# Kernel optimization log

Hardware: AMD Instinct MI355X
Metric: run time of the kernel (lower is better)

Reference implementation:

```python
import jax, jax.numpy as jnp
import numpy as np

N, F = 4096, 256  # nodes, in_features == hidden_features == out_features; num_heads = 1
LN_EPS = 1e-5
L1_EPS = 1e-12


def setup_inputs() -> dict:
    key = jax.random.key(0)
    k0, k1, k2, k3, k4 = jax.random.split(key, 5)
    h = jax.random.normal(k0, (N, F), jnp.float32)
    x = jax.random.normal(k1, (N, F), jnp.float32)
    s = 1.0 / np.sqrt(F)
    s_v = 1.0 / np.sqrt(F + 3)
    # torch Linear weight layout: [out_features, in_features]
    w_k = jax.random.uniform(k2, (F, F), jnp.float32, -s, s)
    w_q = jax.random.uniform(k3, (F, F), jnp.float32, -s, s)
    w_v = jax.random.uniform(k4, (F, F + 3), jnp.float32, -s_v, s_v)
    # mixing init: ones * semantic_weight(-1.0), row 0 zeroed
    mixing = jnp.full((2, 2), -1.0, jnp.float32).at[0].set(0.0)
    ln_gamma = jnp.ones((F,), jnp.float32)
    ln_beta = jnp.zeros((F,), jnp.float32)
    return {"h": h, "x": x, "w_k": w_k, "w_q": w_q, "w_v": w_v,
            "mixing": mixing, "ln_gamma": ln_gamma, "ln_beta": ln_beta}


def reference(h, x, w_k, w_q, w_v, mixing, ln_gamma, ln_beta):
    h0, x0 = h, x
    # LayerNorm (biased variance, eps=1e-5)
    mu = h.mean(-1, keepdims=True)
    var = ((h - mu) ** 2).mean(-1, keepdims=True)
    hn = (h - mu) * jax.lax.rsqrt(var + LN_EPS) * ln_gamma + ln_beta
    # F.normalize(x, p=1): divide by max(L1 norm, eps)
    xn = x / jnp.maximum(jnp.abs(x).sum(-1, keepdims=True), L1_EPS)
    # projections (single head: [N, F])
    k = hn @ w_k.T
    q = hn @ w_q.T
    # feature-attention: softmax over last dim of k q^T / sqrt(F)
    a_h = jax.nn.softmax((k @ q.T) * (F ** -0.5), axis=-1)          # [N, N]
    # x-affinity
    a_x = xn @ xn.T                                                  # [N, N]
    # stats of a_x rows: diag, sum, std (unbiased, ddof=1)
    i = jnp.stack([jnp.diagonal(a_x), a_x.sum(-1), a_x.std(-1, ddof=1)], axis=-1)  # [N, 3]
    # learned 2x2 mixing, softmax over dim 0 (columns)
    m = jax.nn.softmax(mixing, axis=0)
    a_x2 = a_x * m[0, 0] + a_h * m[1, 0]
    a_h2 = a_x * m[0, 1] + a_h * m[1, 1]
    # torch a_h.transpose(-1, 0) swaps the row axis with the head axis,
    # transposing the NxN matrix (head dim = 1): h <- a_h2^T @ hn
    h_agg = a_h2.T @ hn                                              # [N, F]
    x_out = a_x2 @ xn                                                # [N, F]
    h_out = jax.nn.elu(jnp.concatenate([h_agg, i], axis=-1) @ w_v.T)
    return (h_out + h0, x_out + x0)
```

## Files before the change

kernel.cpp:

```cpp
#include <hip/hip_runtime.h>
#include <cstdint>
#include <cstddef>

#define NB 4096
#define FD 256

typedef __attribute__((ext_vector_type(4))) float f32x4;
typedef __attribute__((ext_vector_type(8))) short bf16x8;

__device__ __forceinline__ ushort f2bf(float f) {
  union { float f; uint32_t u; } v; v.f = f;
  uint32_t r = v.u + 0x7fffu + ((v.u >> 16) & 1u);
  return (ushort)(r >> 16);
}
__device__ __forceinline__ float bf2f(ushort b) {
  union { uint32_t u; float f; } v; v.u = ((uint32_t)b) << 16;
  return v.f;
}

__device__ __forceinline__ void gld16(const void* g, void* l) {
  __builtin_amdgcn_global_load_lds(
      (const __attribute__((address_space(1))) char*)g,
      (__attribute__((address_space(3))) char*)l, 16, 0, 0);
}

__device__ __forceinline__ float wave_reduce_sum(float v) {
#pragma unroll
  for (int off = 32; off >= 1; off >>= 1) v += __shfl_xor(v, off);
  return v;
}
__device__ __forceinline__ float wave_reduce_max(float v) {
#pragma unroll
  for (int off = 32; off >= 1; off >>= 1) v = fmaxf(v, __shfl_xor(v, off));
  return v;
}

__global__ __launch_bounds__(256) void rownorm_kernel(
    const float* __restrict__ h, const float* __restrict__ x,
    const float* __restrict__ gamma, const float* __restrict__ beta,
    ushort* __restrict__ hnb, ushort* __restrict__ xnb, float* __restrict__ diag) {
  __shared__ float rA[4], rB[4], rC[4], rD[4];
  const int r = blockIdx.x, t = threadIdx.x, wid = t >> 6, lane = t & 63;
  const size_t base = (size_t)r * FD + t;
  const float hv = h[base], xv = x[base];
  float s1 = wave_reduce_sum(hv);
  float s2 = wave_reduce_sum(hv * hv);
  float a1 = wave_reduce_sum(fabsf(xv));
  float q1 = wave_reduce_sum(xv * xv);
  if (lane == 0) { rA[wid] = s1; rB[wid] = s2; rC[wid] = a1; rD[wid] = q1; }
  __syncthreads();
  const float S1 = rA[0] + rA[1] + rA[2] + rA[3];
  const float S2 = rB[0] + rB[1] + rB[2] + rB[3];
  const float L1 = rC[0] + rC[1] + rC[2] + rC[3];
  const float Q1 = rD[0] + rD[1] + rD[2] + rD[3];
  const float mu = S1 * (1.0f / FD);
  const float var = S2 * (1.0f / FD) - mu * mu;
  const float rstd = rsqrtf(var + 1e-5f);
  const float d = fmaxf(L1, 1e-12f), dinv = 1.0f / d;
  hnb[base] = f2bf((hv - mu) * rstd * gamma[t] + beta[t]);
  xnb[base] = f2bf(xv * dinv);
  if (t == 0) diag[r] = Q1 * dinv * dinv;
}

__global__ __launch_bounds__(256) void wcast_kernel(
    const float* __restrict__ w_k, const float* __restrict__ w_q,
    const float* __restrict__ w_v,
    ushort* __restrict__ wkqb, ushort* __restrict__ wvAb,
    float* __restrict__ wvbT3) {
  const int r = blockIdx.x, t = threadIdx.x;
  wkqb[r * 256 + t] = f2bf(w_k[r * 256 + t]);
  wkqb[(256 + r) * 256 + t] = f2bf(w_q[r * 256 + t]);
  wvAb[r * 256 + t] = f2bf(w_v[(size_t)r * 259 + t]);
  if (t < 3) wvbT3[t * 256 + r] = w_v[(size_t)r * 259 + 256 + t];
}

__global__ __launch_bounds__(256) void transpose2_kernel(
    const ushort* __restrict__ inA, ushort* __restrict__ outA,
    const ushort* __restrict__ inB, ushort* __restrict__ outB, int R, int C) {
  __shared__ ushort tile[64][65];
  const ushort* in = blockIdx.z ? inB : inA;
  ushort* out = blockIdx.z ? outB : outA;
  const int bc = blockIdx.x * 64, br = blockIdx.y * 64;
  const int t = threadIdx.x;
#pragma unroll
  for (int i = 0; i < 16; ++i) {
    const int idx = t + 256 * i;
    const int rr = idx >> 6, cc = idx & 63;
    tile[rr][cc] = in[(size_t)(br + rr) * C + bc + cc];
  }
  __syncthreads();
#pragma unroll
  for (int i = 0; i < 16; ++i) {
    const int idx = t + 256 * i;
    const int rr = idx >> 6, cc = idx & 63;
    out[(size_t)(bc + rr) * R + br + cc] = tile[cc][rr];
  }
}

__global__ __launch_bounds__(256) void transpose_kernel(
    const ushort* __restrict__ in, ushort* __restrict__ out, int R, int C) {
  __shared__ ushort tile[64][65];
  const int bc = blockIdx.x * 64, br = blockIdx.y * 64;
  const int t = threadIdx.x;
#pragma unroll
  for (int i = 0; i < 16; ++i) {
    const int idx = t + 256 * i;
    const int rr = idx >> 6, cc = idx & 63;
    tile[rr][cc] = in[(size_t)(br + rr) * C + bc + cc];
  }
  __syncthreads();
#pragma unroll
  for (int i = 0; i < 16; ++i) {
    const int idx = t + 256 * i;
    const int rr = idx >> 6, cc = idx & 63;
    out[(size_t)(bc + rr) * R + br + cc] = tile[cc][rr];
  }
}

__global__ __launch_bounds__(256) void colsum_kernel(
    const ushort* __restrict__ xnT, float* __restrict__ s) {
  __shared__ float red[4];
  const int f = blockIdx.x, t = threadIdx.x, wid = t >> 6, lane = t & 63;
  float a = 0.f;
#pragma unroll
  for (int i = 0; i < 16; ++i) a += bf2f(xnT[(size_t)f * NB + t + 256 * i]);
  a = wave_reduce_sum(a);
  if (lane == 0) red[wid] = a;
  __syncthreads();
  if (t == 0) s[f] = red[0] + red[1] + red[2] + red[3];
}

__global__ __launch_bounds__(256) void reduce16g_kernel(
    const float* __restrict__ in, ushort* __restrict__ t23B,
    ushort* __restrict__ M2T) {
  const int idx = blockIdx.x * 256 + threadIdx.x;
  const int i = idx >> 9, j = idx & 511;
  float a = 0.f;
#pragma unroll
  for (int z = 0; z < 16; ++z) a += in[(size_t)z * (256 * 512) + idx];
  if (j < 256) t23B[i * 256 + j] = f2bf(a);
  else M2T[i * 256 + (j - 256)] = f2bf(a);
}

__global__ __launch_bounds__(256) void softmax_kernel(
    const ushort* __restrict__ S, ushort* __restrict__ P) {
  __shared__ float red[4];
  const int r = blockIdx.x, t = threadIdx.x, wid = t >> 6, lane = t & 63;
  const uint4* Sr = (const uint4*)(S + (size_t)r * NB);
  float v[16];
  float lmax = -1e30f;
#pragma unroll
  for (int i = 0; i < 2; ++i) {
    const uint4 c = Sr[t + 256 * i];
    const uint32_t w4[4] = {c.x, c.y, c.z, c.w};
#pragma unroll
    for (int j = 0; j < 4; ++j) {
      v[i * 8 + j * 2]     = bf2f((ushort)(w4[j] & 0xffffu));
      v[i * 8 + j * 2 + 1] = bf2f((ushort)(w4[j] >> 16));
    }
  }
#pragma unroll
  for (int u = 0; u < 16; ++u) lmax = fmaxf(lmax, v[u]);
  lmax = wave_reduce_max(lmax);
  if (lane == 0) red[wid] = lmax;
  __syncthreads();
  const float gmax = fmaxf(fmaxf(red[0], red[1]), fmaxf(red[2], red[3]));
  __syncthreads();
  float lsum = 0.f;
#pragma unroll
  for (int u = 0; u < 16; ++u) { v[u] = __expf(v[u] - gmax); lsum += v[u]; }
  lsum = wave_reduce_sum(lsum);
  if (lane == 0) red[wid] = lsum;
  __syncthreads();
  const float pinv = 1.f / (red[0] + red[1] + red[2] + red[3]);
  uint4* Pr = (uint4*)(P + (size_t)r * NB);
#pragma unroll
  for (int i = 0; i < 2; ++i) {
    uint4 o;
    o.x = (uint32_t)f2bf(v[i*8+0] * pinv) | ((uint32_t)f2bf(v[i*8+1] * pinv) << 16);
    o.y = (uint32_t)f2bf(v[i*8+2] * pinv) | ((uint32_t)f2bf(v[i*8+3] * pinv) << 16);
    o.z = (uint32_t)f2bf(v[i*8+4] * pinv) | ((uint32_t)f2bf(v[i*8+5] * pinv) << 16);
    o.w = (uint32_t)f2bf(v[i*8+6] * pinv) | ((uint32_t)f2bf(v[i*8+7] * pinv) << 16);
    Pr[t + 256 * i] = o;
  }
}

__global__ __launch_bounds__(256) void megacombine_kernel(
    const ushort* __restrict__ px, const ushort* __restrict__ ph,
    const float* __restrict__ t23, const ushort* __restrict__ xnb,
    const float* __restrict__ sv, const float* __restrict__ diag,
    const float* __restrict__ x, const float* __restrict__ h,
    const float* __restrict__ wvbT3, const float* __restrict__ mix,
    float* __restrict__ out_x, float* __restrict__ out_h) {
  __shared__ float rA[4], rB[4];
  const size_t NF = (size_t)NB * FD;
  const int i = blockIdx.x, f = threadIdx.x, wid = f >> 6, lane = f & 63;
  const float e0x = __expf(mix[0]), e1x = __expf(mix[2]);
  const float mAx = e0x / (e0x + e1x), mBx = e1x / (e0x + e1x);
  const float e0h = __expf(mix[1]), e1h = __expf(mix[3]);
  const float mAh = e0h / (e0h + e1h), mBh = e1h / (e0h + e1h);

  const size_t rowoff = (size_t)i * FD + f;
  float ax = 0.f, ah = 0.f;
#pragma unroll
  for (int z = 0; z < 8; ++z) {
    ax += bf2f(px[(size_t)z * NF + rowoff]);
    ah += bf2f(ph[(size_t)z * NF + rowoff]);
  }
  const float t2v = t23[(size_t)i * 512 + f];
  const float t3v = t23[(size_t)i * 512 + 256 + f];
  const float xv = bf2f(xnb[rowoff]);

  float rs = wave_reduce_sum(xv * sv[f]);
  float rq = wave_reduce_sum(xv * t2v);
  if (lane == 0) { rA[wid] = rs; rB[wid] = rq; }
  __syncthreads();
  rs = rA[0] + rA[1] + rA[2] + rA[3];
  rq = rB[0] + rB[1] + rB[2] + rB[3];
  const float mean = rs * (1.0f / NB);
  const float var = (rq - (float)NB * mean * mean) * (1.0f / (NB - 1));
  const float sd = sqrtf(fmaxf(var, 0.f));
  const float dg = diag[i];
  const float statsterm = dg * wvbT3[f] + rs * wvbT3[256 + f] + sd * wvbT3[512 + f];

  out_x[rowoff] = mBx * ax + mAx * t2v + x[rowoff];
  const float pre = mBh * ah + mAh * t3v + statsterm;
  out_h[rowoff] = ((pre > 0.f) ? pre : expm1f(pre)) + h[rowoff];
}

template <int BM, int BN, int EPI>
__global__ __launch_bounds__(256) void gemm_nt(
    const ushort* __restrict__ A, int lda,
    const ushort* __restrict__ B, int ldb,
    void* __restrict__ Cp, int ldc, int K, float alpha,
    size_t pstride) {
  constexpr int WAVES_N = (BM <= 32) ? 4 : 2;
  constexpr int WAVES_M = 4 / WAVES_N;
  constexpr int WM = BM / WAVES_M, WN = BN / WAVES_N;
  constexpr int MR = WM / 16, NR = WN / 16;
  __shared__ __align__(16) ushort At[2][BM][32];
  __shared__ __align__(16) ushort Bt[2][BN][32];
  const int tid = threadIdx.x;
  const int wave = tid >> 6, lane = tid & 63;
  const int wr = wave / WAVES_N, wc = wave % WAVES_N;

  const int gx = gridDim.x, gy = gridDim.y;
  const int nwg = gx * gy * gridDim.z;
  int flat = blockIdx.x + gx * (blockIdx.y + gy * blockIdx.z);
  if ((nwg & 7) == 0) flat = (flat & 7) * (nwg >> 3) + (flat >> 3);
  const int bx = flat % gx, by = (flat / gx) % gy, bz = flat / (gx * gy);

  const int bi = by * BM, bj = bx * BN;
  const int fr = lane & 15, fq = lane >> 4;
  const int sub = lane >> 2, q = lane & 3;

  f32x4 acc[MR][NR];
#pragma unroll
  for (int m = 0; m < MR; ++m)
#pragma unroll
    for (int n = 0; n < NR; ++n) acc[m][n] = (f32x4){0.f, 0.f, 0.f, 0.f};

  const int kbase = (EPI >= 5) ? bz * K : 0;
  const int kend = kbase + K;

  auto stage = [&](int bufi, int k0) {
    for (int c = wave; c < BM / 16; c += 4) {
      const int row = c * 16 + sub;
      const int qs = q ^ (row & 3);
      gld16(A + (size_t)(bi + row) * lda + k0 + qs * 8, &At[bufi][c * 16][0]);
    }
    for (int c = wave; c < BN / 16; c += 4) {
      const int row = c * 16 + sub;
      const int qs = q ^ (row & 3);
      gld16(B + (size_t)(bj + row) * ldb + k0 + qs * 8, &Bt[bufi][c * 16][0]);
    }
  };

  stage(0, kbase);
  __syncthreads();

  int cur = 0;
  for (int k0 = kbase; k0 < kend; k0 += 32) {
    if (k0 + 32 < kend) stage(cur ^ 1, k0 + 32);
    bf16x8 a[MR], b[NR];
#pragma unroll
    for (int m = 0; m < MR; ++m) {
      const int row = wr * WM + m * 16 + fr;
      a[m] = *(const bf16x8*)((const char*)&At[cur][row][0] + ((fq ^ (row & 3)) * 16));
    }
#pragma unroll
    for (int n = 0; n < NR; ++n) {
      const int row = wc * WN + n * 16 + fr;
      b[n] = *(const bf16x8*)((const char*)&Bt[cur][row][0] + ((fq ^ (row & 3)) * 16));
    }
#pragma unroll
    for (int m = 0; m < MR; ++m)
#pragma unroll
      for (int n = 0; n < NR; ++n)
        acc[m][n] = __builtin_amdgcn_mfma_f32_16x16x32_bf16(a[m], b[n], acc[m][n], 0, 0, 0);
    __syncthreads();
    cur ^= 1;
  }

#pragma unroll
  for (int m = 0; m < MR; ++m)
#pragma unroll
    for (int n = 0; n < NR; ++n)
#pragma unroll
      for (int r = 0; r < 4; ++r) {
        const int row = bi + wr * WM + m * 16 + fq * 4 + r;
        const int col = bj + wc * WN + n * 16 + fr;
        const size_t ci = (size_t)row * ldc + col;
        const float v = acc[m][n][r];
        if (EPI == 0) ((float*)Cp)[ci] = v * alpha;
        else if (EPI == 1) ((ushort*)Cp)[ci] = f2bf(v * alpha);
        else if (EPI == 5) ((float*)Cp)[(size_t)bz * pstride + ci] = v;
        else if (EPI == 6) ((ushort*)Cp)[(size_t)bz * pstride + ci] = f2bf(v);
      }
}

extern "C" void kernel_launch(void* const* d_in, const int* in_sizes, int n_in,
                              void* d_out, int out_size, void* d_ws, size_t ws_size,
                              hipStream_t stream) {
  const float* h      = (const float*)d_in[0];
  const float* x      = (const float*)d_in[1];
  const float* w_k    = (const float*)d_in[2];
  const float* w_q    = (const float*)d_in[3];
  const float* w_v    = (const float*)d_in[4];
  const float* mixing = (const float*)d_in[5];
  const float* gamma  = (const float*)d_in[6];
  const float* beta   = (const float*)d_in[7];

  float* out_h = (float*)d_out;
  float* out_x = out_h + (size_t)NB * FD;

  char* w = (char*)d_ws;
  ushort* S     = (ushort*)(w + 0);
  ushort* P     = (ushort*)(w + 33554432);
  ushort* PT    = (ushort*)(w + 67108864);
  ushort* hnb   = (ushort*)(w + 100663296);
  ushort* xnb   = (ushort*)(w + 102760448);
  ushort* xnbT  = (ushort*)(w + 104857600);
  ushort* hnbT  = (ushort*)(w + 106954752);
  ushort* kq    = (ushort*)(w + 109051904);
  ushort* hvT   = (ushort*)(w + 113246208);
  float*  t23   = (float*)(w + 115343360);
  ushort* t23B  = (ushort*)(w + 123731968);
  ushort* M2T   = (ushort*)(w + 123994112);
  ushort* wkqb  = (ushort*)(w + 124125184);
  ushort* wvAb  = (ushort*)(w + 124387328);
  float*  wvbT3 = (float*)(w + 124518400);
  float*  diag  = (float*)(w + 124521472);
  float*  sv    = (float*)(w + 124537856);
  float*  Gramp = (float*)(w + 67108864);
  ushort* px    = (ushort*)(w + 0);
  ushort* ph    = (ushort*)(w + 16777216);

  rownorm_kernel<<<NB, 256, 0, stream>>>(h, x, gamma, beta, hnb, xnb, diag);
  wcast_kernel<<<FD, 256, 0, stream>>>(w_k, w_q, w_v, wkqb, wvAb, wvbT3);
  transpose2_kernel<<<dim3(FD / 64, NB / 64, 2), 256, 0, stream>>>(
      xnb, xnbT, hnb, hnbT, NB, FD);
  colsum_kernel<<<FD, 256, 0, stream>>>(xnbT, sv);

  gemm_nt<64, 64, 1><<<dim3(512 / 64, NB / 64), 256, 0, stream>>>(
      hnb, FD, wkqb, FD, kq, 512, FD, 1.f, 0);

  gemm_nt<64, 64, 5><<<dim3(512 / 64, 256 / 64, 16), 256, 0, stream>>>(
      xnbT, NB, xnbT, NB, Gramp, 512, NB / 16, 1.f, (size_t)256 * 512);
  reduce16g_kernel<<<256 * 512 / 256, 256, 0, stream>>>(Gramp, t23B, M2T);

  gemm_nt<64, 64, 1><<<dim3(4, 4), 256, 0, stream>>>(
      wvAb, FD, M2T, FD, t23B + 256 * 256, FD, FD, 1.f, 0);

  gemm_nt<64, 64, 1><<<dim3(NB / 64, FD / 64), 256, 0, stream>>>(
      wvAb, FD, hnb, FD, hvT, NB, FD, 1.f, 0);

  gemm_nt<64, 64, 0><<<dim3(512 / 64, NB / 64), 256, 0, stream>>>(
      xnb, FD, t23B, FD, t23, 512, FD, 1.f, 0);

  gemm_nt<128, 128, 1><<<dim3(NB / 128, NB / 128), 256, 0, stream>>>(
      kq, 512, kq + 256, 512, S, NB, FD, 0.0625f, 0);
  softmax_kernel<<<NB, 256, 0, stream>>>(S, P);
  transpose_kernel<<<dim3(NB / 64, NB / 64), 256, 0, stream>>>(P, PT, NB, NB);

  gemm_nt<128, 128, 6><<<dim3(FD / 128, NB / 128, 8), 256, 0, stream>>>(
      P, NB, xnbT, NB, px, FD, NB / 8, 1.f, (size_t)NB * FD);
  gemm_nt<128, 128, 6><<<dim3(FD / 128, NB / 128, 8), 256, 0, stream>>>(
      PT, NB, hvT, NB, ph, FD, NB / 8, 1.f, (size_t)NB * FD);

  megacombine_kernel<<<NB, 256, 0, stream>>>(
      px, ph, t23, xnb, sv, diag, x, h, wvbT3, mixing, out_x, out_h);
}
```

Measured before the change: 140.8 us.

## Fuse softmax with transpose and batch three independent GEMMs into one launch

Replaces the separate softmax and 4096x4096 transpose kernels with one kernel that handles 16 rows per block. It writes P directly and writes PT through a small LDS tile, so the extra read and write of P for the transpose goes away. The kernel makes three passes over S (max, sum, write) and has only 256 blocks with a barrier on every column tile, so it may expose latency. It also merges the kq projection, the Gram partials and the hvT GEMM into one grouped launch with interleaved block mapping, which cuts launch overhead and fills the GPU better.

```diff
diff --git a/kernel.cpp b/kernel.cpp
--- a/kernel.cpp
+++ b/kernel.cpp
@@ -27,11 +27,6 @@
 __device__ __forceinline__ float wave_reduce_sum(float v) {
 #pragma unroll
   for (int off = 32; off >= 1; off >>= 1) v += __shfl_xor(v, off);
-  return v;
-}
-__device__ __forceinline__ float wave_reduce_max(float v) {
-#pragma unroll
-  for (int off = 32; off >= 1; off >>= 1) v = fmaxf(v, __shfl_xor(v, off));
   return v;
 }
 
@@ -97,26 +92,6 @@
   }
 }
 
-__global__ __launch_bounds__(256) void transpose_kernel(
-    const ushort* __restrict__ in, ushort* __restrict__ out, int R, int C) {
-  __shared__ ushort tile[64][65];
-  const int bc = blockIdx.x * 64, br = blockIdx.y * 64;
-  const int t = threadIdx.x;
-#pragma unroll
-  for (int i = 0; i < 16; ++i) {
-    const int idx = t + 256 * i;
-    const int rr = idx >> 6, cc = idx & 63;
-    tile[rr][cc] = in[(size_t)(br + rr) * C + bc + cc];
-  }
-  __syncthreads();
-#pragma unroll
-  for (int i = 0; i < 16; ++i) {
-    const int idx = t + 256 * i;
-    const int rr = idx >> 6, cc = idx & 63;
-    out[(size_t)(bc + rr) * R + br + cc] = tile[cc][rr];
-  }
-}
-
 __global__ __launch_bounds__(256) void colsum_kernel(
     const ushort* __restrict__ xnT, float* __restrict__ s) {
   __shared__ float red[4];
@@ -142,46 +117,67 @@
   else M2T[i * 256 + (j - 256)] = f2bf(a);
 }
 
-__global__ __launch_bounds__(256) void softmax_kernel(
-    const ushort* __restrict__ S, ushort* __restrict__ P) {
-  __shared__ float red[4];
-  const int r = blockIdx.x, t = threadIdx.x, wid = t >> 6, lane = t & 63;
-  const uint4* Sr = (const uint4*)(S + (size_t)r * NB);
-  float v[16];
-  float lmax = -1e30f;
-#pragma unroll
-  for (int i = 0; i < 2; ++i) {
-    const uint4 c = Sr[t + 256 * i];
-    const uint32_t w4[4] = {c.x, c.y, c.z, c.w};
+__global__ __launch_bounds__(256) void softmax_t_kernel(
+    const ushort* __restrict__ S, ushort* __restrict__ P,
+    ushort* __restrict__ PT) {
+  __shared__ ushort tile[16][66];
+  const int t = threadIdx.x;
+  const int rl = t >> 4, sub = t & 15;
+  const int r0 = blockIdx.x * 16;
+  const ushort* Srow = S + (size_t)(r0 + rl) * NB;
+  ushort* Prow = P + (size_t)(r0 + rl) * NB;
+
+  float m = -1e30f;
+  for (int c = sub * 8; c < NB; c += 128) {
+    const uint4 cc = *(const uint4*)(Srow + c);
+    const uint32_t w4[4] = {cc.x, cc.y, cc.z, cc.w};
 #pragma unroll
     for (int j = 0; j < 4; ++j) {
-      v[i * 8 + j * 2]     = bf2f((ushort)(w4[j] & 0xffffu));
-      v[i * 8 + j * 2 + 1] = bf2f((ushort)(w4[j] >> 16));
-    }
-  }
-#pragma unroll
-  for (int u = 0; u < 16; ++u) lmax = fmaxf(lmax, v[u]);
-  lmax = wave_reduce_max(lmax);
-  if (lane == 0) red[wid] = lmax;
-  __syncthreads();
-  const float gmax = fmaxf(fmaxf(red[0], red[1]), fmaxf(red[2], red[3]));
-  __syncthreads();
-  float lsum = 0.f;
-#pragma unroll
-  for (int u = 0; u < 16; ++u) { v[u] = __expf(v[u] - gmax); lsum += v[u]; }
-  lsum = wave_reduce_sum(lsum);
-  if (lane == 0) red[wid] = lsum;
-  __syncthreads();
-  const float pinv = 1.f / (red[0] + red[1] + red[2] + red[3]);
-  uint4* Pr = (uint4*)(P + (size_t)r * NB);
-#pragma unroll
-  for (int i = 0; i < 2; ++i) {
-    uint4 o;
-    o.x = (uint32_t)f2bf(v[i*8+0] * pinv) | ((uint32_t)f2bf(v[i*8+1] * pinv) << 16);
-    o.y = (uint32_t)f2bf(v[i*8+2] * pinv) | ((uint32_t)f2bf(v[i*8+3] * pinv) << 16);
-    o.z = (uint32_t)f2bf(v[i*8+4] * pinv) | ((uint32_t)f2bf(v[i*8+5] * pinv) << 16);
-    o.w = (uint32_t)f2bf(v[i*8+6] * pinv) | ((uint32_t)f2bf(v[i*8+7] * pinv) << 16);
-    Pr[t + 256 * i] = o;
+      m = fmaxf(m, bf2f((ushort)(w4[j] & 0xffffu)));
+      m = fmaxf(m, bf2f((ushort)(w4[j] >> 16)));
+    }
+  }
+  m = fmaxf(m, __shfl_xor(m, 1));
+  m = fmaxf(m, __shfl_xor(m, 2));
+  m = fmaxf(m, __shfl_xor(m, 4));
+  m = fmaxf(m, __shfl_xor(m, 8));
+
+  float s = 0.f;
+  for (int c = sub * 8; c < NB; c += 128) {
+    const uint4 cc = *(const uint4*)(Srow + c);
+    const uint32_t w4[4] = {cc.x, cc.y, cc.z, cc.w};
+#pragma unroll
+    for (int j = 0; j < 4; ++j) {
+      s += __expf(bf2f((ushort)(w4[j] & 0xffffu)) - m);
+      s += __expf(bf2f((ushort)(w4[j] >> 16)) - m);
+    }
+  }
+  s += __shfl_xor(s, 1);
+  s += __shfl_xor(s, 2);
+  s += __shfl_xor(s, 4);
+  s += __shfl_xor(s, 8);
+  const float pinv = 1.f / s;
+
+  const int jj = t >> 2;
+  const int ii = (t & 3) * 4;
+  for (int ct = 0; ct < 64; ++ct) {
+    const int c = ct * 64 + sub * 4;
+    const ushort4 sv = *(const ushort4*)(Srow + c);
+    ushort4 o;
+    o.x = f2bf(__expf(bf2f(sv.x) - m) * pinv);
+    o.y = f2bf(__expf(bf2f(sv.y) - m) * pinv);
+    o.z = f2bf(__expf(bf2f(sv.z) - m) * pinv);
+    o.w = f2bf(__expf(bf2f(sv.w) - m) * pinv);
+    *(ushort4*)(Prow + c) = o;
+    *(ushort4*)(&tile[rl][sub * 4]) = o;
+    __syncthreads();
+    ushort4 ot;
+    ot.x = tile[ii + 0][jj];
+    ot.y = tile[ii + 1][jj];
+    ot.z = tile[ii + 2][jj];
+    ot.w = tile[ii + 3][jj];
+    *(ushort4*)(PT + (size_t)(ct * 64 + jj) * NB + r0 + ii) = ot;
+    __syncthreads();
   }
 }
 
@@ -226,6 +222,96 @@
   out_x[rowoff] = mBx * ax + mAx * t2v + x[rowoff];
   const float pre = mBh * ah + mAh * t3v + statsterm;
   out_h[rowoff] = ((pre > 0.f) ? pre : expm1f(pre)) + h[rowoff];
+}
+
+struct GDesc {
+  const ushort* A; const ushort* B; void* C;
+  int lda, ldb, ldc, K, gx, gy, epi;
+  float alpha; long pstride; int nb;
+};
+
+__global__ __launch_bounds__(256) void gemm_batch3(
+    GDesc d0, GDesc d1, GDesc d2, int ntot) {
+  int flat = blockIdx.x;
+  flat = (flat & 7) * (ntot >> 3) + (flat >> 3);
+  GDesc d; int l;
+  if (flat < d0.nb) { d = d0; l = flat; }
+  else if (flat < d0.nb + d1.nb) { d = d1; l = flat - d0.nb; }
+  else { d = d2; l = flat - d0.nb - d1.nb; }
+  const int bx = l % d.gx;
+  const int rest = l / d.gx;
+  const int by = rest % d.gy, bz = rest / d.gy;
+
+  __shared__ __align__(16) ushort At[2][64][32];
+  __shared__ __align__(16) ushort Bt[2][64][32];
+  const int tid = threadIdx.x;
+  const int wave = tid >> 6, lane = tid & 63;
+  const int wr = wave >> 1, wc = wave & 1;
+  const int bi = by * 64, bj = bx * 64;
+  const int fr = lane & 15, fq = lane >> 4;
+  const int sub = lane >> 2, q = lane & 3;
+
+  f32x4 acc[2][2];
+#pragma unroll
+  for (int m = 0; m < 2; ++m)
+#pragma unroll
+    for (int n = 0; n < 2; ++n) acc[m][n] = (f32x4){0.f, 0.f, 0.f, 0.f};
+
+  const int kbase = bz * d.K;
+  const int kend = kbase + d.K;
+
+  auto stage = [&](int bufi, int k0) {
+    {
+      const int row = wave * 16 + sub;
+      const int qs = q ^ (row & 3);
+      gld16(d.A + (size_t)(bi + row) * d.lda + k0 + qs * 8, &At[bufi][wave * 16][0]);
+    }
+    {
+      const int row = wave * 16 + sub;
+      const int qs = q ^ (row & 3);
+      gld16(d.B + (size_t)(bj + row) * d.ldb + k0 + qs * 8, &Bt[bufi][wave * 16][0]);
+    }
+  };
+
+  stage(0, kbase);
+  __syncthreads();
+
+  int cur = 0;
+  for (int k0 = kbase; k0 < kend; k0 += 32) {
+    if (k0 + 32 < kend) stage(cur ^ 1, k0 + 32);
+    bf16x8 a[2], b[2];
+#pragma unroll
+    for (int m = 0; m < 2; ++m) {
+      const int row = wr * 32 + m * 16 + fr;
+      a[m] = *(const bf16x8*)((const char*)&At[cur][row][0] + ((fq ^ (row & 3)) * 16));
+    }
+#pragma unroll
+    for (int n = 0; n < 2; ++n) {
+      const int row = wc * 32 + n * 16 + fr;
+      b[n] = *(const bf16x8*)((const char*)&Bt[cur][row][0] + ((fq ^ (row & 3)) * 16));
+    }
+#pragma unroll
+    for (int m = 0; m < 2; ++m)
+#pragma unroll
+      for (int n = 0; n < 2; ++n)
+        acc[m][n] = __builtin_amdgcn_mfma_f32_16x16x32_bf16(a[m], b[n], acc[m][n], 0, 0, 0);
+    __syncthreads();
+    cur ^= 1;
+  }
+
+#pragma unroll
+  for (int m = 0; m < 2; ++m)
+#pragma unroll
+    for (int n = 0; n < 2; ++n)
+#pragma unroll
+      for (int r = 0; r < 4; ++r) {
+        const int row = bi + wr * 32 + m * 16 + fq * 4 + r;
+        const int col = bj + wc * 32 + n * 16 + fr;
+        const size_t ci = (size_t)row * d.ldc + col;
+        const float v = acc[m][n][r];
+        if (d.epi == 1) ((ushort*)d.C)[ci] = f2bf(v * d.alpha);
+        else ((float*)d.C)[(size_t)bz * d.pstride + ci] = v;
+      }
 }
 
 template <int BM, int BN, int EPI>
@@ -362,26 +448,25 @@
       xnb, xnbT, hnb, hnbT, NB, FD);
   colsum_kernel<<<FD, 256, 0, stream>>>(xnbT, sv);
 
-  gemm_nt<64, 64, 1><<<dim3(512 / 64, NB / 64), 256, 0, stream>>>(
-      hnb, FD, wkqb, FD, kq, 512, FD, 1.f, 0);
-
-  gemm_nt<64, 64, 5><<<dim3(512 / 64, 256 / 64, 16), 256, 0, stream>>>(
-      xnbT, NB, xnbT, NB, Gramp, 512, NB / 16, 1.f, (size_t)256 * 512);
+  {
+    GDesc dkq = {hnb, wkqb, kq, FD, FD, 512, FD, 8, 64, 1, 1.f, 0, 512};
+    GDesc dgr = {xnbT, xnbT, Gramp, NB, NB, 512, NB / 16, 8, 4, 5, 1.f,
+                 (long)(256 * 512), 512};
+    GDesc dhv = {wvAb, hnb, hvT, FD, FD, NB, FD, 64, 4, 1, 1.f, 0, 256};
+    gemm_batch3<<<1280, 256, 0, stream>>>(dkq, dgr, dhv, 1280);
+  }
   reduce16g_kernel<<<256 * 512 / 256, 256, 0, stream>>>(Gramp, t23B, M2T);
 
   gemm_nt<64, 64, 1><<<dim3(4, 4), 256, 0, stream>>>(
       wvAb, FD, M2T, FD, t23B + 256 * 256, FD, FD, 1.f, 0);
 
-  gemm_nt<64, 64, 1><<<dim3(NB / 64, FD / 64), 256, 0, stream>>>(
-      wvAb, FD, hnb, FD, hvT, NB, FD, 1.f, 0);
-
   gemm_nt<64, 64, 0><<<dim3(512 / 64, NB / 64), 256, 0, stream>>>(
       xnb, FD, t23B, FD, t23, 512, FD, 1.f, 0);
 
   gemm_nt<128, 128, 1><<<dim3(NB / 128, NB / 128), 256, 0, stream>>>(
       kq, 512, kq + 256, 512, S, NB, FD, 0.0625f, 0);
-  softmax_kernel<<<NB, 256, 0, stream>>>(S, P);
-  transpose_kernel<<<dim3(NB / 64, NB / 64), 256, 0, stream>>>(P, PT, NB, NB);
+
+  softmax_t_kernel<<<NB / 16, 256, 0, stream>>>(S, P, PT);
 
   gemm_nt<128, 128, 6><<<dim3(FD / 128, NB / 128, 8), 256, 0, stream>>>(
       P, NB, xnbT, NB, px, FD, NB / 8, 1.f, (size_t)NB * FD);
```

After: 168.0 us. 19.3% more time.
